# Performance work log

Measured on AMD Instinct MI355X. Metric: run time of the kernel, lower is better.

## Reference

```python
import jax, jax.numpy as jnp
import numpy as np

N, Q, D = 8, 900, 256
HB, WB = 200, 200
L, NH, P = 6, 8, 4
HD = D // NH
FF = 512
NCLS, NBOX = 10, 8
ODIM = NCLS + NBOX
THRESH = 0.5
OFFSET_SCALE = 1.0
SCALE = 1.0 / float(np.sqrt(HD))


def _ln(x, g, b, eps=1e-5):
    m = jnp.mean(x, axis=-1, keepdims=True)
    v = jnp.mean((x - m) ** 2, axis=-1, keepdims=True)
    return (x - m) * jax.lax.rsqrt(v + eps) * g + b


def _mha(x, Wq, bq, Wk, bk, Wv, bv, Wo, bo):
    q = (x @ Wq + bq).reshape(N, Q, NH, HD)
    k = (x @ Wk + bk).reshape(N, Q, NH, HD)
    v = (x @ Wv + bv).reshape(N, Q, NH, HD)
    att = jax.nn.softmax(jnp.einsum('bqhd,bkhd->bhqk', q, k) * SCALE, axis=-1)
    o = jnp.einsum('bhqk,bkhd->bqhd', att, v).reshape(N, Q, D)
    return o @ Wo + bo


def _deform(q, ref, bev, dv_W, dv_b, off_W, off_b, aw_W, aw_b, do_W, do_b):
    # value projection of BEV map: (N, HW, D) -> (N, NH, HW, HD)
    val = (bev @ dv_W + dv_b).reshape(N, HB * WB, NH, HD).transpose(0, 2, 1, 3)
    off = (q @ off_W + off_b).reshape(N, Q, NH, P, 2)
    aw = jax.nn.softmax((q @ aw_W + aw_b).reshape(N, Q, NH, P), axis=-1)
    # ref: (N,Q,1,2) pixel coords -> broadcast to (N,Q,NH,P,2)
    loc = ref[:, :, :, None, :] + off * OFFSET_SCALE
    x = jnp.clip(loc[..., 0], 0.0, WB - 1.0)
    y = jnp.clip(loc[..., 1], 0.0, HB - 1.0)
    x0 = jnp.floor(x)
    y0 = jnp.floor(y)
    x1 = jnp.minimum(x0 + 1.0, WB - 1.0)
    y1 = jnp.minimum(y0 + 1.0, HB - 1.0)
    wx = (x - x0).transpose(0, 2, 1, 3)[..., None]  # (N,NH,Q,P,1)
    wy = (y - y0).transpose(0, 2, 1, 3)[..., None]

    def gather(ix, iy):
        idx = (iy * WB + ix).astype(jnp.int32)               # (N,Q,NH,P)
        idx = idx.transpose(0, 2, 1, 3).reshape(N, NH, Q * P, 1)
        g = jnp.take_along_axis(val, idx, axis=2)            # (N,NH,Q*P,HD)
        return g.reshape(N, NH, Q, P, HD)

    samp = (gather(x0, y0) * (1 - wx) * (1 - wy)
            + gather(x1, y0) * wx * (1 - wy)
            + gather(x0, y1) * (1 - wx) * wy
            + gather(x1, y1) * wx * wy)                      # (N,NH,Q,P,HD)
    awt = aw.transpose(0, 2, 1, 3)                           # (N,NH,Q,P)
    out = jnp.einsum('bhqp,bhqpd->bqhd', awt, samp).reshape(N, Q, D)
    return out @ do_W + do_b


def _ref_points():
    # n_sample=Q points evenly spread over the HBxWB grid, pixel coords, unnormalized
    idx = jnp.round(jnp.linspace(0.0, HB * WB - 1.0, Q)).astype(jnp.int32)
    x = (idx % WB).astype(jnp.float32)
    y = (idx // WB).astype(jnp.float32)
    rp = jnp.stack([x, y], axis=-1)                          # (Q,2)
    return jnp.broadcast_to(rp[None, :, None, :], (N, Q, 1, 2))


def _det(x, W1, b1, W2, b2):
    h = jax.nn.relu(x @ W1 + b1)
    o = h @ W2 + b2
    return jnp.concatenate([jax.nn.sigmoid(o[..., :NCLS]), o[..., NCLS:]], axis=-1)


def setup_inputs() -> dict:
    key = jax.random.key(0)
    ks = iter(jax.random.split(key, 48))

    def w(shape, s=0.02):
        return jax.random.normal(next(ks), shape, jnp.float32) * s

    inp = {
        'bev_features': jax.random.normal(next(ks), (N, HB * WB, D), jnp.float32),
        'pos_emb': w((Q, D), 1.0),
        'Wq': w((L, D, D)), 'bq': jnp.zeros((L, D), jnp.float32),
        'Wk': w((L, D, D)), 'bk': jnp.zeros((L, D), jnp.float32),
        'Wv': w((L, D, D)), 'bv': jnp.zeros((L, D), jnp.float32),
        'Wo': w((L, D, D)), 'bo': jnp.zeros((L, D), jnp.float32),
        'ln1_g': jnp.ones((L, D), jnp.float32), 'ln1_b': jnp.zeros((L, D), jnp.float32),
        'ln2_g': jnp.ones((L, D), jnp.float32), 'ln2_b': jnp.zeros((L, D), jnp.float32),
        'ln3_g': jnp.ones((L, D), jnp.float32), 'ln3_b': jnp.zeros((L, D), jnp.float32),
        'dv_W': w((L, D, D)), 'dv_b': jnp.zeros((L, D), jnp.float32),
        'off_W': w((L, D, NH * P * 2), 0.01), 'off_b': jnp.zeros((L, NH * P * 2), jnp.float32),
        'aw_W': w((L, D, NH * P), 0.01), 'aw_b': jnp.zeros((L, NH * P), jnp.float32),
        'do_W': w((L, D, D)), 'do_b': jnp.zeros((L, D), jnp.float32),
        'f1_W': w((L, D, FF)), 'f1_b': jnp.zeros((L, FF), jnp.float32),
        'f2_W': w((L, FF, D)), 'f2_b': jnp.zeros((L, D), jnp.float32),
        'det_W1': w((D, D)), 'det_b1': jnp.zeros((D,), jnp.float32),
        'det_W2': w((D, ODIM)), 'det_b2': jnp.zeros((ODIM,), jnp.float32),
    }
    return inp


def reference(bev_features, pos_emb, Wq, bq, Wk, bk, Wv, bv, Wo, bo,
              ln1_g, ln1_b, ln2_g, ln2_b, ln3_g, ln3_b,
              dv_W, dv_b, off_W, off_b, aw_W, aw_b, do_W, do_b,
              f1_W, f1_b, f2_W, f2_b, det_W1, det_b1, det_W2, det_b2):
    queries = jnp.broadcast_to(pos_emb[None], (N, Q, D))
    ref = _ref_points()
    output = queries
    layer_results = []
    for i in range(L):
        x = output + queries
        a = _mha(x, Wq[i], bq[i], Wk[i], bk[i], Wv[i], bv[i], Wo[i], bo[i])
        x2 = _ln(x + a, ln1_g[i], ln1_b[i])
        d = _deform(x2, ref, bev_features, dv_W[i], dv_b[i], off_W[i], off_b[i],
                    aw_W[i], aw_b[i], do_W[i], do_b[i])
        x3 = _ln(x2 + d, ln2_g[i], ln2_b[i])
        f = jax.nn.relu(x3 @ f1_W[i] + f1_b[i]) @ f2_W[i] + f2_b[i]
        output = _ln(x3 + f, ln3_g[i], ln3_b[i])
        layer_results.append(_det(output, det_W1, det_b1, det_W2, det_b2))
    layer_results = jnp.stack(layer_results, axis=0)   # (L,N,Q,ODIM)
    detections = layer_results[-1]
    track_mask = detections[..., 0] >= THRESH
    return output, detections, track_mask, layer_results
```

## Files before the change

kernel.cpp:

```cpp
#include <hip/hip_runtime.h>
#include <hip/hip_bf16.h>
#include <math.h>

#define N 8
#define Q 900
#define D 256
#define HB 200
#define WB 200
#define L 6
#define NH 8
#define P 4
#define HD 32
#define FF 512
#define NCLS 10
#define ODIM 18
#define HW (HB*WB)
#define NQ (N*Q)
#define NQD (NQ*D)
#define QD (Q*D)
#define SCALE 0.17677669529663687f

typedef __attribute__((ext_vector_type(4))) float f32x4;
typedef __attribute__((ext_vector_type(8))) short short8v;

__device__ __forceinline__ short bf16_of(float f) {
  __hip_bfloat16 h = __float2bfloat16(f);
  return __builtin_bit_cast(short, h);
}

#define TM 64
#define TN 64
#define KC 128

template <int ACT>
__global__ __launch_bounds__(256) void gemm_kernel(
    const float* __restrict__ A, const float* __restrict__ B,
    const float* __restrict__ bias, float* __restrict__ C,
    int M, int K, int Nc) {
  __shared__ float AsT[KC][TM + 4];
  __shared__ float Bs[KC][TN + 4];
  const int tid = threadIdx.x;
  const int tx = tid & 15, ty = tid >> 4;
  const int m0 = blockIdx.x * TM, n0 = blockIdx.y * TN;

  float c[4][4] = {};

  for (int kc = 0; kc < K; kc += KC) {
    {
      int r = tid >> 2;
      int gr = m0 + r;
      int kb = (tid & 3) * 32;
#pragma unroll
      for (int q = 0; q < 8; ++q) {
        int k = kb + q * 4;
        float4 av = make_float4(0.f, 0.f, 0.f, 0.f);
        if (gr < M) av = *(const float4*)(A + (size_t)gr * K + kc + k);
        AsT[k + 0][r] = av.x; AsT[k + 1][r] = av.y;
        AsT[k + 2][r] = av.z; AsT[k + 3][r] = av.w;
      }
    }
    {
#pragma unroll
      for (int i = 0; i < 8; ++i) {
        int idx = i * 256 + tid;
        int kr = idx >> 4;
        int c4 = (idx & 15) * 4;
        *(float4*)&Bs[kr][c4] = *(const float4*)(B + (size_t)(kc + kr) * Nc + n0 + c4);
      }
    }
    __syncthreads();
#pragma unroll 8
    for (int kk = 0; kk < KC; ++kk) {
      float4 av = *(const float4*)&AsT[kk][ty * 4];
      float4 bv = *(const float4*)&Bs[kk][tx * 4];
      c[0][0] += av.x * bv.x; c[0][1] += av.x * bv.y; c[0][2] += av.x * bv.z; c[0][3] += av.x * bv.w;
      c[1][0] += av.y * bv.x; c[1][1] += av.y * bv.y; c[1][2] += av.y * bv.z; c[1][3] += av.y * bv.w;
      c[2][0] += av.z * bv.x; c[2][1] += av.z * bv.y; c[2][2] += av.z * bv.z; c[2][3] += av.z * bv.w;
      c[3][0] += av.w * bv.x; c[3][1] += av.w * bv.y; c[3][2] += av.w * bv.z; c[3][3] += av.w * bv.w;
    }
    __syncthreads();
  }

#pragma unroll
  for (int i = 0; i < 4; ++i) {
    int row = m0 + ty * 4 + i;
    if (row >= M) continue;
#pragma unroll
    for (int j = 0; j < 4; ++j) {
      int col = n0 + tx * 4 + j;
      float v = c[i][j] + bias[col];
      if (ACT == 1) v = fmaxf(v, 0.f);
      C[(size_t)row * Nc + col] = v;
    }
  }
}

__global__ __launch_bounds__(256) void gemm_qkv_kernel(
    const float* __restrict__ outp, const float* __restrict__ pos,
    const float* __restrict__ Wq, const float* __restrict__ bq,
    const float* __restrict__ Wk, const float* __restrict__ bk,
    const float* __restrict__ Wv, const float* __restrict__ bv,
    unsigned short* __restrict__ Oq, unsigned short* __restrict__ Ok,
    unsigned short* __restrict__ Ov) {
  __shared__ float AsT[KC][TM + 4];
  __shared__ float Bs[KC][TN + 4];
  const int tid = threadIdx.x;
  const int tx = tid & 15, ty = tid >> 4;
  const int m0 = blockIdx.x * TM;
  const int wsel = blockIdx.y >> 2;
  const int n0 = (blockIdx.y & 3) * TN;
  const float* B = (wsel == 0) ? Wq : (wsel == 1) ? Wk : Wv;
  const float* bias = (wsel == 0) ? bq : (wsel == 1) ? bk : bv;
  unsigned short* C = (wsel == 0) ? Oq : (wsel == 1) ? Ok : Ov;

  float c[4][4] = {};

  for (int kc = 0; kc < D; kc += KC) {
    {
      int r = tid >> 2;
      int gr = m0 + r;
      int kb = (tid & 3) * 32;
      const float* ar = outp + (size_t)gr * D + kc;
      const float* pr = pos + (size_t)(gr % Q) * D + kc;
#pragma unroll
      for (int q = 0; q < 8; ++q) {
        int k = kb + q * 4;
        float4 av = make_float4(0.f, 0.f, 0.f, 0.f);
        if (gr < NQ) {
          float4 ov = *(const float4*)(ar + k);
          float4 pv = *(const float4*)(pr + k);
          av.x = ov.x + pv.x; av.y = ov.y + pv.y; av.z = ov.z + pv.z; av.w = ov.w + pv.w;
        }
        AsT[k + 0][r] = av.x; AsT[k + 1][r] = av.y;
        AsT[k + 2][r] = av.z; AsT[k + 3][r] = av.w;
      }
    }
    {
#pragma unroll
      for (int i = 0; i < 8; ++i) {
        int idx = i * 256 + tid;
        int kr = idx >> 4;
        int c4 = (idx & 15) * 4;
        *(float4*)&Bs[kr][c4] = *(const float4*)(B + (size_t)(kc + kr) * D + n0 + c4);
      }
    }
    __syncthreads();
#pragma unroll 8
    for (int kk = 0; kk < KC; ++kk) {
      float4 av = *(const float4*)&AsT[kk][ty * 4];
      float4 bv4 = *(const float4*)&Bs[kk][tx * 4];
      c[0][0] += av.x * bv4.x; c[0][1] += av.x * bv4.y; c[0][2] += av.x * bv4.z; c[0][3] += av.x * bv4.w;
      c[1][0] += av.y * bv4.x; c[1][1] += av.y * bv4.y; c[1][2] += av.y * bv4.z; c[1][3] += av.y * bv4.w;
      c[2][0] += av.z * bv4.x; c[2][1] += av.z * bv4.y; c[2][2] += av.z * bv4.z; c[2][3] += av.z * bv4.w;
      c[3][0] += av.w * bv4.x; c[3][1] += av.w * bv4.y; c[3][2] += av.w * bv4.z; c[3][3] += av.w * bv4.w;
    }
    __syncthreads();
  }

#pragma unroll
  for (int i = 0; i < 4; ++i) {
    int row = m0 + ty * 4 + i;
    if (row >= NQ) continue;
    ushort4 o4;
    o4.x = (unsigned short)bf16_of(c[i][0] + bias[n0 + tx * 4 + 0]);
    o4.y = (unsigned short)bf16_of(c[i][1] + bias[n0 + tx * 4 + 1]);
    o4.z = (unsigned short)bf16_of(c[i][2] + bias[n0 + tx * 4 + 2]);
    o4.w = (unsigned short)bf16_of(c[i][3] + bias[n0 + tx * 4 + 3]);
    *(ushort4*)(C + (size_t)row * D + n0 + tx * 4) = o4;
  }
}

#define TMT 64
template <int ACT>
__global__ __launch_bounds__(256) void gemm_thin_kernel(
    const float* __restrict__ A, const float* __restrict__ B,
    const float* __restrict__ bias, float* __restrict__ C,
    int M, int K, int Nc) {
  __shared__ float AsT[KC][TMT + 4];
  __shared__ float Bs[KC][16 + 2];
  const int tid = threadIdx.x;
  const int tx = tid & 15, ty = tid >> 4;
  const int m0 = blockIdx.x * TMT, n0 = blockIdx.y * 16;

  float c[4] = {};

  for (int kc = 0; kc < K; kc += KC) {
    {
      int r = tid >> 2;
      int gr = m0 + r;
      int kb = (tid & 3) * 32;
#pragma unroll
      for (int q = 0; q < 8; ++q) {
        int k = kb + q * 4;
        float4 av = make_float4(0.f, 0.f, 0.f, 0.f);
        if (gr < M) av = *(const float4*)(A + (size_t)gr * K + kc + k);
        AsT[k + 0][r] = av.x; AsT[k + 1][r] = av.y;
        AsT[k + 2][r] = av.z; AsT[k + 3][r] = av.w;
      }
    }
    {
#pragma unroll
      for (int i = 0; i < 8; ++i) {
        int idx = i * 256 + tid;
        int kr = idx >> 4;
        int cc = idx & 15;
        int gc = n0 + cc;
        Bs[kr][cc] = (gc < Nc) ? B[(size_t)(kc + kr) * Nc + gc] : 0.f;
      }
    }
    __syncthreads();
#pragma unroll 8
    for (int kk = 0; kk < KC; ++kk) {
      float4 av = *(const float4*)&AsT[kk][ty * 4];
      float bv = Bs[kk][tx];
      c[0] += av.x * bv; c[1] += av.y * bv; c[2] += av.z * bv; c[3] += av.w * bv;
    }
    __syncthreads();
  }

  int col = n0 + tx;
  if (col < Nc) {
    float bs = bias[col];
#pragma unroll
    for (int i = 0; i < 4; ++i) {
      int row = m0 + ty * 4 + i;
      if (row < M) {
        float v = c[i] + bs;
        if (ACT == 2 && col < NCLS) v = 1.f / (1.f + expf(-v));
        C[(size_t)row * Nc + col] = v;
      }
    }
  }
}

__global__ __launch_bounds__(256) void gemm_offaw_kernel(
    const float* __restrict__ A,
    const float* __restrict__ offW, const float* __restrict__ offb,
    const float* __restrict__ awW, const float* __restrict__ awb,
    float* __restrict__ offC, float* __restrict__ awC) {
  __shared__ float AsT[KC][TMT + 4];
  __shared__ float Bs[KC][16 + 2];
  const int tid = threadIdx.x;
  const int tx = tid & 15, ty = tid >> 4;
  const int m0 = blockIdx.x * TMT;
  const bool isOff = blockIdx.y < 4;
  const int n0 = isOff ? blockIdx.y * 16 : (blockIdx.y - 4) * 16;
  const int Nc = isOff ? 64 : 32;
  const float* B = isOff ? offW : awW;
  const float* bias = isOff ? offb : awb;
  float* C = isOff ? offC : awC;

  float c[4] = {};

  for (int kc = 0; kc < D; kc += KC) {
    {
      int r = tid >> 2;
      int gr = m0 + r;
      int kb = (tid & 3) * 32;
#pragma unroll
      for (int q = 0; q < 8; ++q) {
        int k = kb + q * 4;
        float4 av = make_float4(0.f, 0.f, 0.f, 0.f);
        if (gr < NQ) av = *(const float4*)(A + (size_t)gr * D + kc + k);
        AsT[k + 0][r] = av.x; AsT[k + 1][r] = av.y;
        AsT[k + 2][r] = av.z; AsT[k + 3][r] = av.w;
      }
    }
    {
#pragma unroll
      for (int i = 0; i < 8; ++i) {
        int idx = i * 256 + tid;
        int kr = idx >> 4;
        int cc = idx & 15;
        Bs[kr][cc] = B[(size_t)(kc + kr) * Nc + n0 + cc];
      }
    }
    __syncthreads();
#pragma unroll 8
    for (int kk = 0; kk < KC; ++kk) {
      float4 av = *(const float4*)&AsT[kk][ty * 4];
      float bv = Bs[kk][tx];
      c[0] += av.x * bv; c[1] += av.y * bv; c[2] += av.z * bv; c[3] += av.w * bv;
    }
    __syncthreads();
  }

  int col = n0 + tx;
  float bs = bias[col];
#pragma unroll
  for (int i = 0; i < 4; ++i) {
    int row = m0 + ty * 4 + i;
    if (row < NQ) C[(size_t)row * Nc + col] = c[i] + bs;
  }
}

__global__ __launch_bounds__(256) void attn_kernel(
    const unsigned short* __restrict__ qg, const unsigned short* __restrict__ kg,
    const unsigned short* __restrict__ vg, float* __restrict__ og) {
  const int n = blockIdx.z, h = blockIdx.y;
  const int wv = threadIdx.x >> 6;
  const int lane = threadIdx.x & 63;
  const int g = lane >> 4;
  const int c = lane & 15;
  const int q0 = blockIdx.x * 64 + wv * 16;

  const unsigned short* qb = qg + (size_t)n * Q * D + h * HD;
  const unsigned short* kb = kg + (size_t)n * Q * D + h * HD;
  const unsigned short* vb = vg + (size_t)n * Q * D + h * HD;

  short8v qf = {};
  {
    int qr = q0 + c;
    if (qr < Q) qf = *(const short8v*)(qb + (size_t)qr * D + g * 8);
  }

  const float SC2 = SCALE * 1.4426950408889634f;
  float m2 = -1e30f, l = 0.f;
  f32x4 acc0 = {0.f, 0.f, 0.f, 0.f}, acc1 = {0.f, 0.f, 0.f, 0.f};

  for (int kt0 = 0; kt0 < Q; kt0 += 64) {
    float s[16];
#pragma unroll
    for (int t = 0; t < 4; ++t) {
      short8v kf = {};
      int kr = kt0 + t * 16 + c;
      if (kr < Q) kf = *(const short8v*)(kb + (size_t)kr * D + g * 8);
      f32x4 d = __builtin_amdgcn_mfma_f32_16x16x32_bf16(kf, qf, (f32x4){0.f, 0.f, 0.f, 0.f}, 0, 0, 0);
#pragma unroll
      for (int r = 0; r < 4; ++r) s[t * 4 + r] = d[r];
    }
#pragma unroll
    for (int t = 0; t < 4; ++t)
#pragma unroll
      for (int r = 0; r < 4; ++r) {
        int key = kt0 + t * 16 + g * 4 + r;
        s[t * 4 + r] = (key < Q) ? s[t * 4 + r] * SC2 : -1e30f;
      }
    float tm = s[0];
#pragma unroll
    for (int j = 1; j < 16; ++j) tm = fmaxf(tm, s[j]);
    tm = fmaxf(tm, __shfl_xor(tm, 16));
    tm = fmaxf(tm, __shfl_xor(tm, 32));
    float m2n = fmaxf(m2, tm);
    float corr = exp2f(m2 - m2n);
    m2 = m2n;
    float ps = 0.f;
#pragma unroll
    for (int j = 0; j < 16; ++j) { s[j] = exp2f(s[j] - m2); ps += s[j]; }
    ps += __shfl_xor(ps, 16);
    ps += __shfl_xor(ps, 32);
    l = l * corr + ps;
    float cr0 = __shfl(corr, g * 4 + 0);
    float cr1 = __shfl(corr, g * 4 + 1);
    float cr2 = __shfl(corr, g * 4 + 2);
    float cr3 = __shfl(corr, g * 4 + 3);
    acc0[0] *= cr0; acc0[1] *= cr1; acc0[2] *= cr2; acc0[3] *= cr3;
    acc1[0] *= cr0; acc1[1] *= cr1; acc1[2] *= cr2; acc1[3] *= cr3;

#pragma unroll
    for (int pr = 0; pr < 2; ++pr) {
      short8v pa, v0 = {}, v1 = {};
#pragma unroll
      for (int j = 0; j < 8; ++j) pa[j] = bf16_of(s[pr * 8 + j]);
#pragma unroll
      for (int j = 0; j < 8; ++j) {
        int key = kt0 + (pr * 2 + (j >> 2)) * 16 + g * 4 + (j & 3);
        if (key < Q) {
          const unsigned short* vp = vb + (size_t)key * D;
          v0[j] = (short)vp[c];
          v1[j] = (short)vp[c + 16];
        }
      }
      acc0 = __builtin_amdgcn_mfma_f32_16x16x32_bf16(pa, v0, acc0, 0, 0, 0);
      acc1 = __builtin_amdgcn_mfma_f32_16x16x32_bf16(pa, v1, acc1, 0, 0, 0);
    }
  }

  float inv = 1.f / l;
  float iv[4];
#pragma unroll
  for (int r = 0; r < 4; ++r) iv[r] = __shfl(inv, g * 4 + r);
#pragma unroll
  for (int r = 0; r < 4; ++r) {
    int qr = q0 + g * 4 + r;
    if (qr < Q) {
      float* op = og + (size_t)(n * Q + qr) * D + h * HD;
      op[c] = acc0[r] * iv[r];
      op[c + 16] = acc1[r] * iv[r];
    }
  }
}

__global__ __launch_bounds__(256) void ln_add_kernel(
    const float* __restrict__ A, const float* __restrict__ Bp,
    const float* __restrict__ g, const float* __restrict__ b,
    float* __restrict__ out) {
  const int wave = threadIdx.x >> 6;
  const int lane = threadIdx.x & 63;
  const int row = blockIdx.x * 4 + wave;
  const size_t base = (size_t)row * D + lane * 4;
  float4 a4 = *(const float4*)(A + base);
  float4 b4 = *(const float4*)(Bp + base);
  float v0 = a4.x + b4.x, v1 = a4.y + b4.y, v2 = a4.z + b4.z, v3 = a4.w + b4.w;
  float sum = v0 + v1 + v2 + v3;
#pragma unroll
  for (int off = 1; off < 64; off <<= 1) sum += __shfl_xor(sum, off);
  float mean = sum * (1.f / D);
  float d0 = v0 - mean, d1 = v1 - mean, d2 = v2 - mean, d3 = v3 - mean;
  float vsum = d0 * d0 + d1 * d1 + d2 * d2 + d3 * d3;
#pragma unroll
  for (int off = 1; off < 64; off <<= 1) vsum += __shfl_xor(vsum, off);
  float inv_std = 1.0f / sqrtf(vsum * (1.f / D) + 1e-5f);
  float4 g4 = *(const float4*)(g + lane * 4);
  float4 bb4 = *(const float4*)(b + lane * 4);
  float4 o4;
  o4.x = d0 * inv_std * g4.x + bb4.x;
  o4.y = d1 * inv_std * g4.y + bb4.y;
  o4.z = d2 * inv_std * g4.z + bb4.z;
  o4.w = d3 * inv_std * g4.w + bb4.w;
  *(float4*)(out + base) = o4;
}

__global__ __launch_bounds__(256) void ln_add3_kernel(
    const float* __restrict__ A, const float* __restrict__ pos,
    const float* __restrict__ Bp,
    const float* __restrict__ g, const float* __restrict__ b,
    float* __restrict__ out) {
  const int wave = threadIdx.x >> 6;
  const int lane = threadIdx.x & 63;
  const int row = blockIdx.x * 4 + wave;
  const size_t base = (size_t)row * D + lane * 4;
  const size_t pbase = (size_t)(row % Q) * D + lane * 4;
  float4 a4 = *(const float4*)(A + base);
  float4 p4 = *(const float4*)(pos + pbase);
  float4 b4 = *(const float4*)(Bp + base);
  float x0 = a4.x + p4.x, x1 = a4.y + p4.y, x2 = a4.z + p4.z, x3 = a4.w + p4.w;
  float v0 = x0 + b4.x, v1 = x1 + b4.y, v2 = x2 + b4.z, v3 = x3 + b4.w;
  float sum = v0 + v1 + v2 + v3;
#pragma unroll
  for (int off = 1; off < 64; off <<= 1) sum += __shfl_xor(sum, off);
  float mean = sum * (1.f / D);
  float d0 = v0 - mean, d1 = v1 - mean, d2 = v2 - mean, d3 = v3 - mean;
  float vsum = d0 * d0 + d1 * d1 + d2 * d2 + d3 * d3;
#pragma unroll
  for (int off = 1; off < 64; off <<= 1) vsum += __shfl_xor(vsum, off);
  float inv_std = 1.0f / sqrtf(vsum * (1.f / D) + 1e-5f);
  float4 g4 = *(const float4*)(g + lane * 4);
  float4 bb4 = *(const float4*)(b + lane * 4);
  float4 o4;
  o4.x = d0 * inv_std * g4.x + bb4.x;
  o4.y = d1 * inv_std * g4.y + bb4.y;
  o4.z = d2 * inv_std * g4.z + bb4.z;
  o4.w = d3 * inv_std * g4.w + bb4.w;
  *(float4*)(out + base) = o4;
}

__global__ __launch_bounds__(256) void deform_kernel(
    const float* __restrict__ bev, const float* __restrict__ offB,
    const float* __restrict__ awB, const float* __restrict__ dvW,
    const float* __restrict__ dvb, float* __restrict__ dtmp) {
  const int bq0 = blockIdx.x * 4;
  const int n = bq0 / Q;
  const int t = threadIdx.x;

  __shared__ float aw_s[4][NH * P];
  __shared__ int   idx_s[4][NH * P * 4];
  __shared__ float w_s[4][NH * P * 4];
  __shared__ float agg_s[4][NH][D];
  __shared__ float red_s[4][4][D];

  if (t < 128) {
    int qq = t >> 5, e = t & 31;
    int bq = bq0 + qq;
    int qi = bq - n * Q;
    float tq = __fmul_rn((float)qi, 44.492767333984375f);
    int ir = (int)rintf(tq);
    float rx = (float)(ir % WB);
    float ry = (float)(ir / WB);
    float ox = offB[(size_t)bq * 64 + e * 2 + 0];
    float oy = offB[(size_t)bq * 64 + e * 2 + 1];
    float lx = fminf(fmaxf(rx + ox, 0.f), (float)(WB - 1));
    float ly = fminf(fmaxf(ry + oy, 0.f), (float)(HB - 1));
    float x0 = floorf(lx), y0 = floorf(ly);
    float x1 = fminf(x0 + 1.f, (float)(WB - 1));
    float y1 = fminf(y0 + 1.f, (float)(HB - 1));
    float wx = lx - x0, wy = ly - y0;
    int b4 = e * 4;
    idx_s[qq][b4 + 0] = (int)y0 * WB + (int)x0; w_s[qq][b4 + 0] = (1.f - wx) * (1.f - wy);
    idx_s[qq][b4 + 1] = (int)y0 * WB + (int)x1; w_s[qq][b4 + 1] = wx * (1.f - wy);
    idx_s[qq][b4 + 2] = (int)y1 * WB + (int)x0; w_s[qq][b4 + 2] = (1.f - wx) * wy;
    idx_s[qq][b4 + 3] = (int)y1 * WB + (int)x1; w_s[qq][b4 + 3] = wx * wy;
  } else if (t < 160) {
    int idx = t - 128;
    int qq = idx >> 3, hh = idx & 7;
    const float* ap = awB + (size_t)(bq0 + qq) * 32 + hh * P;
    float l0 = ap[0], l1 = ap[1], l2 = ap[2], l3 = ap[3];
    float mx = fmaxf(fmaxf(l0, l1), fmaxf(l2, l3));
    float e0 = expf(l0 - mx), e1 = expf(l1 - mx), e2 = expf(l2 - mx), e3 = expf(l3 - mx);
    float inv = 1.f / (e0 + e1 + e2 + e3);
    aw_s[qq][hh * P + 0] = e0 * inv; aw_s[qq][hh * P + 1] = e1 * inv;
    aw_s[qq][hh * P + 2] = e2 * inv; aw_s[qq][hh * P + 3] = e3 * inv;
  }
  __syncthreads();

  {
    const float* bevn = bev + (size_t)n * HW * D;
    const int wv = t >> 6, lane = t & 63;
    const int c4 = lane * 4;
#pragma unroll
    for (int u = 0; u < 8; ++u) {
      int pid = wv + u * 4;
      int qq = pid >> 3, h = pid & 7;
      f32x4 acc = {0.f, 0.f, 0.f, 0.f};
#pragma unroll
      for (int p = 0; p < P; ++p) {
        int e = h * P + p;
        float aw = aw_s[qq][e];
        const int* ix = &idx_s[qq][e * 4];
        const float* wsp = &w_s[qq][e * 4];
        float4 g0 = *(const float4*)(bevn + (size_t)ix[0] * D + c4);
        float4 g1 = *(const float4*)(bevn + (size_t)ix[1] * D + c4);
        float4 g2 = *(const float4*)(bevn + (size_t)ix[2] * D + c4);
        float4 g3 = *(const float4*)(bevn + (size_t)ix[3] * D + c4);
        acc[0] += aw * (wsp[0] * g0.x + wsp[1] * g1.x + wsp[2] * g2.x + wsp[3] * g3.x);
        acc[1] += aw * (wsp[0] * g0.y + wsp[1] * g1.y + wsp[2] * g2.y + wsp[3] * g3.y);
        acc[2] += aw * (wsp[0] * g0.z + wsp[1] * g1.z + wsp[2] * g2.z + wsp[3] * g3.z);
        acc[3] += aw * (wsp[0] * g0.w + wsp[1] * g1.w + wsp[2] * g2.w + wsp[3] * g3.w);
      }
      *(f32x4*)&agg_s[qq][h][c4] = acc;
    }
  }
  __syncthreads();

  {
    const int chunk = t >> 6;
    const int col4 = t & 63;
    const int tt0 = col4 * 4;
    const int h = tt0 >> 5;
    f32x4 p[4] = {{0.f,0.f,0.f,0.f},{0.f,0.f,0.f,0.f},{0.f,0.f,0.f,0.f},{0.f,0.f,0.f,0.f}};
#pragma unroll 4
    for (int dd4 = 0; dd4 < 64; dd4 += 4) {
      int dd = chunk * 64 + dd4;
      float4 w0 = *(const float4*)(dvW + (size_t)(dd + 0) * D + tt0);
      float4 w1 = *(const float4*)(dvW + (size_t)(dd + 1) * D + tt0);
      float4 w2 = *(const float4*)(dvW + (size_t)(dd + 2) * D + tt0);
      float4 w3 = *(const float4*)(dvW + (size_t)(dd + 3) * D + tt0);
#pragma unroll
      for (int qq = 0; qq < 4; ++qq) {
        float4 a = *(const float4*)&agg_s[qq][h][dd];
        p[qq][0] += a.x * w0.x + a.y * w1.x + a.z * w2.x + a.w * w3.x;
        p[qq][1] += a.x * w0.y + a.y * w1.y + a.z * w2.y + a.w * w3.y;
        p[qq][2] += a.x * w0.z + a.y * w1.z + a.z * w2.z + a.w * w3.z;
        p[qq][3] += a.x * w0.w + a.y * w1.w + a.z * w2.w + a.w * w3.w;
      }
    }
#pragma unroll
    for (int qq = 0; qq < 4; ++qq) *(f32x4*)&red_s[qq][chunk][tt0] = p[qq];
  }
  __syncthreads();
  {
    float bs = dvb[t];
#pragma unroll
    for (int qq = 0; qq < 4; ++qq) {
      dtmp[(size_t)(bq0 + qq) * D + t] =
          bs + red_s[qq][0][t] + red_s[qq][1][t] + red_s[qq][2][t] + red_s[qq][3][t];
    }
  }
}

__global__ void bcast_q_kernel(const float* __restrict__ pos, float* __restrict__ out) {
  for (size_t i = (size_t)blockIdx.x * blockDim.x + threadIdx.x; i < (size_t)NQD;
       i += (size_t)gridDim.x * blockDim.x)
    out[i] = pos[i % QD];
}
__global__ void finalize_kernel(const float* __restrict__ lr5, float* __restrict__ det,
                                float* __restrict__ mask) {
  int i = blockIdx.x * blockDim.x + threadIdx.x;
  if (i < NQ * ODIM) det[i] = lr5[i];
  if (i < NQ) mask[i] = (lr5[(size_t)i * ODIM] >= 0.5f) ? 1.0f : 0.0f;
}

extern "C" void kernel_launch(void* const* d_in, const int* in_sizes, int n_in,
                              void* d_out, int out_size, void* d_ws, size_t ws_size,
                              hipStream_t stream) {
  const float* bev  = (const float*)d_in[0];
  const float* pos  = (const float*)d_in[1];
  const float* Wq   = (const float*)d_in[2];  const float* bq  = (const float*)d_in[3];
  const float* Wk   = (const float*)d_in[4];  const float* bk  = (const float*)d_in[5];
  const float* Wv   = (const float*)d_in[6];  const float* bv  = (const float*)d_in[7];
  const float* Wo   = (const float*)d_in[8];  const float* bo  = (const float*)d_in[9];
  const float* ln1g = (const float*)d_in[10]; const float* ln1b = (const float*)d_in[11];
  const float* ln2g = (const float*)d_in[12]; const float* ln2b = (const float*)d_in[13];
  const float* ln3g = (const float*)d_in[14]; const float* ln3b = (const float*)d_in[15];
  const float* dvW  = (const float*)d_in[16]; const float* dvb = (const float*)d_in[17];
  const float* offW = (const float*)d_in[18]; const float* offb = (const float*)d_in[19];
  const float* awW  = (const float*)d_in[20]; const float* awb = (const float*)d_in[21];
  const float* doW  = (const float*)d_in[22]; const float* dob = (const float*)d_in[23];
  const float* f1W  = (const float*)d_in[24]; const float* f1b = (const float*)d_in[25];
  const float* f2W  = (const float*)d_in[26]; const float* f2b = (const float*)d_in[27];
  const float* dW1  = (const float*)d_in[28]; const float* db1 = (const float*)d_in[29];
  const float* dW2  = (const float*)d_in[30]; const float* db2 = (const float*)d_in[31];

  float* w = (float*)d_ws;
  float* b0 = w + 0 * (size_t)NQD;
  float* b1 = w + 1 * (size_t)NQD;
  float* b2 = w + 2 * (size_t)NQD;
  float* b3 = w + 3 * (size_t)NQD;
  float* ffh = b1;
  float* offB = b0;
  float* awB  = b0 + (size_t)NQ * 64;
  unsigned short* qb16 = (unsigned short*)b1;
  unsigned short* kb16 = (unsigned short*)b1 + NQD;
  unsigned short* vb16 = (unsigned short*)b2;

  float* out_output = (float*)d_out;
  float* out_det    = out_output + (size_t)NQD;
  float* out_mask   = out_det + (size_t)NQ * ODIM;
  float* out_lr     = out_mask + (size_t)NQ;

  const dim3 blk256(256);
  const dim3 qkvGrid((NQ + TM - 1) / TM, 12);
  const dim3 gemmGridD((NQ + TM - 1) / TM, D / TN);
  const dim3 gemmGridFF((NQ + TM - 1) / TM, FF / TN);
  const dim3 offawGrid((NQ + TMT - 1) / TMT, 6);
  const dim3 thinGridDet((NQ + TMT - 1) / TMT, 2);
  const dim3 attnGrid((Q + 63) / 64, NH, N);
  const dim3 lnGrid(NQ / 4);
  const dim3 defGrid(NQ / 4);
  const int ewGrid = 1024;

  bcast_q_kernel<<<ewGrid, blk256, 0, stream>>>(pos, out_output);

  for (int i = 0; i < L; ++i) {
    const size_t wDD = (size_t)i * D * D;
    gemm_qkv_kernel<<<qkvGrid, blk256, 0, stream>>>(out_output, pos,
        Wq + wDD, bq + (size_t)i * D, Wk + wDD, bk + (size_t)i * D,
        Wv + wDD, bv + (size_t)i * D, qb16, kb16, vb16);
    attn_kernel<<<attnGrid, blk256, 0, stream>>>(qb16, kb16, vb16, b0);
    gemm_kernel<0><<<gemmGridD, blk256, 0, stream>>>(b0, Wo + wDD, bo + (size_t)i * D, b1, NQ, D, D);
    ln_add3_kernel<<<lnGrid, blk256, 0, stream>>>(out_output, pos, b1,
        ln1g + (size_t)i * D, ln1b + (size_t)i * D, b2);
    gemm_offaw_kernel<<<offawGrid, blk256, 0, stream>>>(b2,
        offW + (size_t)i * D * 64, offb + (size_t)i * 64,
        awW + (size_t)i * D * 32, awb + (size_t)i * 32, offB, awB);
    deform_kernel<<<defGrid, blk256, 0, stream>>>(bev, offB, awB, dvW + wDD, dvb + (size_t)i * D, b3);
    gemm_kernel<0><<<gemmGridD, blk256, 0, stream>>>(b3, doW + wDD, dob + (size_t)i * D, b1, NQ, D, D);
    ln_add_kernel<<<lnGrid, blk256, 0, stream>>>(b2, b1, ln2g + (size_t)i * D, ln2b + (size_t)i * D, b0);
    gemm_kernel<1><<<gemmGridFF, blk256, 0, stream>>>(b0, f1W + (size_t)i * D * FF, f1b + (size_t)i * FF, ffh, NQ, D, FF);
    gemm_kernel<0><<<gemmGridD, blk256, 0, stream>>>(ffh, f2W + (size_t)i * FF * D, f2b + (size_t)i * D, b3, NQ, FF, D);
    ln_add_kernel<<<lnGrid, blk256, 0, stream>>>(b0, b3, ln3g + (size_t)i * D, ln3b + (size_t)i * D, out_output);
    gemm_kernel<1><<<gemmGridD, blk256, 0, stream>>>(out_output, dW1, db1, b1, NQ, D, D);
    gemm_thin_kernel<2><<<thinGridDet, blk256, 0, stream>>>(b1, dW2, db2, out_lr + (size_t)i * NQ * ODIM, NQ, D, ODIM);
  }

  finalize_kernel<<<(NQ * ODIM + 255) / 256, blk256, 0, stream>>>(out_lr + (size_t)(L - 1) * NQ * ODIM,
                                                                  out_det, out_mask);
}
```

Measured before the change: 2.418 ms.

## Split deform into gather and per-head projection GEMM; shrink attention blocks

The deformable sampling kernel no longer does the value projection in shared memory. It writes per-head aggregated BEV features to a new workspace buffer, and a separate tiled GEMM kernel then applies the per-head slice of the value projection. This is meant to relieve the large shared-memory footprint and the weak projection loop of the fused kernel. The cost is an extra global round trip of an NQ×NH×D buffer and one extra launch. The attention kernel also moves from 256-thread blocks of four waves to single-wave blocks to give more blocks and better occupancy.

```diff
diff --git a/kernel.cpp b/kernel.cpp
--- a/kernel.cpp
+++ b/kernel.cpp
@@ -294,15 +294,70 @@
   }
 }
 
-__global__ __launch_bounds__(256) void attn_kernel(
+__global__ __launch_bounds__(256) void dproj_kernel(
+    const float* __restrict__ agg, const float* __restrict__ dvW,
+    const float* __restrict__ dvb, float* __restrict__ dtmp) {
+  __shared__ float AsT[KC][TMT + 4];
+  __shared__ float Bs[KC][16 + 2];
+  const int tid = threadIdx.x;
+  const int tx = tid & 15, ty = tid >> 4;
+  const int m0 = blockIdx.x * TMT;
+  const int n0 = blockIdx.y * 16;
+  const int h = blockIdx.z;
+  const int ldA = NH * D;
+
+  float c[4] = {};
+
+  for (int kc = 0; kc < D; kc += KC) {
+    {
+      int r = tid >> 2;
+      int gr = m0 + r;
+      int kb = (tid & 3) * 32;
+#pragma unroll
+      for (int q = 0; q < 8; ++q) {
+        int k = kb + q * 4;
+        float4 av = make_float4(0.f, 0.f, 0.f, 0.f);
+        if (gr < NQ) av = *(const float4*)(agg + (size_t)gr * ldA + h * D + kc + k);
+        AsT[k + 0][r] = av.x; AsT[k + 1][r] = av.y;
+        AsT[k + 2][r] = av.z; AsT[k + 3][r] = av.w;
+      }
+    }
+    {
+#pragma unroll
+      for (int i = 0; i < 8; ++i) {
+        int idx = i * 256 + tid;
+        int kr = idx >> 4;
+        int cc = idx & 15;
+        Bs[kr][cc] = dvW[(size_t)(kc + kr) * D + h * HD + n0 + cc];
+      }
+    }
+    __syncthreads();
+#pragma unroll 8
+    for (int kk = 0; kk < KC; ++kk) {
+      float4 av = *(const float4*)&AsT[kk][ty * 4];
+      float bv = Bs[kk][tx];
+      c[0] += av.x * bv; c[1] += av.y * bv; c[2] += av.z * bv; c[3] += av.w * bv;
+    }
+    __syncthreads();
+  }
+
+  int col = h * HD + n0 + tx;
+  float bs = dvb[col];
+#pragma unroll
+  for (int i = 0; i < 4; ++i) {
+    int row = m0 + ty * 4 + i;
+    if (row < NQ) dtmp[(size_t)row * D + col] = c[i] + bs;
+  }
+}
+
+__global__ __launch_bounds__(64) void attn_kernel(
     const unsigned short* __restrict__ qg, const unsigned short* __restrict__ kg,
     const unsigned short* __restrict__ vg, float* __restrict__ og) {
   const int n = blockIdx.z, h = blockIdx.y;
-  const int wv = threadIdx.x >> 6;
-  const int lane = threadIdx.x & 63;
+  const int lane = threadIdx.x;
   const int g = lane >> 4;
   const int c = lane & 15;
-  const int q0 = blockIdx.x * 64 + wv * 16;
+  const int q0 = blockIdx.x * 16;
 
   const unsigned short* qb = qg + (size_t)n * Q * D + h * HD;
   const unsigned short* kb = kg + (size_t)n * Q * D + h * HD;
@@ -455,10 +510,9 @@
   *(float4*)(out + base) = o4;
 }
 
-__global__ __launch_bounds__(256) void deform_kernel(
+__global__ __launch_bounds__(256) void deform_gather_kernel(
     const float* __restrict__ bev, const float* __restrict__ offB,
-    const float* __restrict__ awB, const float* __restrict__ dvW,
-    const float* __restrict__ dvb, float* __restrict__ dtmp) {
+    const float* __restrict__ awB, float* __restrict__ agg) {
   const int bq0 = blockIdx.x * 4;
   const int n = bq0 / Q;
   const int t = threadIdx.x;
@@ -466,8 +520,6 @@
   __shared__ float aw_s[4][NH * P];
   __shared__ int   idx_s[4][NH * P * 4];
   __shared__ float w_s[4][NH * P * 4];
-  __shared__ float agg_s[4][NH][D];
-  __shared__ float red_s[4][4][D];
 
   if (t < 128) {
     int qq = t >> 5, e = t & 31;
@@ -527,43 +579,7 @@
         acc[2] += aw * (wsp[0] * g0.z + wsp[1] * g1.z + wsp[2] * g2.z + wsp[3] * g3.z);
         acc[3] += aw * (wsp[0] * g0.w + wsp[1] * g1.w + wsp[2] * g2.w + wsp[3] * g3.w);
       }
-      *(f32x4*)&agg_s[qq][h][c4] = acc;
-    }
-  }
-  __syncthreads();
-
-  {
-    const int chunk = t >> 6;
-    const int col4 = t & 63;
-    const int tt0 = col4 * 4;
-    const int h = tt0 >> 5;
-    f32x4 p[4] = {{0.f,0.f,0.f,0.f},{0.f,0.f,0.f,0.f},{0.f,0.f,0.f,0.f},{0.f,0.f,0.f,0.f}};
-#pragma unroll 4
-    for (int dd4 = 0; dd4 < 64; dd4 += 4) {
-      int dd = chunk * 64 + dd4;
-      float4 w0 = *(const float4*)(dvW + (size_t)(dd + 0) * D + tt0);
-      float4 w1 = *(const float4*)(dvW + (size_t)(dd + 1) * D + tt0);
-      float4 w2 = *(const float4*)(dvW + (size_t)(dd + 2) * D + tt0);
-      float4 w3 = *(const float4*)(dvW + (size_t)(dd + 3) * D + tt0);
-#pragma unroll
-      for (int qq = 0; qq < 4; ++qq) {
-        float4 a = *(const float4*)&agg_s[qq][h][dd];
-        p[qq][0] += a.x * w0.x + a.y * w1.x + a.z * w2.x + a.w * w3.x;
-        p[qq][1] += a.x * w0.y + a.y * w1.y + a.z * w2.y + a.w * w3.y;
-        p[qq][2] += a.x * w0.z + a.y * w1.z + a.z * w2.z + a.w * w3.z;
-        p[qq][3] += a.x * w0.w + a.y * w1.w + a.z * w2.w + a.w * w3.w;
-      }
-    }
-#pragma unroll
-    for (int qq = 0; qq < 4; ++qq) *(f32x4*)&red_s[qq][chunk][tt0] = p[qq];
-  }
-  __syncthreads();
-  {
-    float bs = dvb[t];
-#pragma unroll
-    for (int qq = 0; qq < 4; ++qq) {
-      dtmp[(size_t)(bq0 + qq) * D + t] =
-          bs + red_s[qq][0][t] + red_s[qq][1][t] + red_s[qq][2][t] + red_s[qq][3][t];
+      *(f32x4*)(agg + ((size_t)(bq0 + qq) * NH + h) * D + c4) = acc;
     }
   }
 }
@@ -606,6 +622,7 @@
   float* b1 = w + 1 * (size_t)NQD;
   float* b2 = w + 2 * (size_t)NQD;
   float* b3 = w + 3 * (size_t)NQD;
+  float* agg = w + 4 * (size_t)NQD;
   float* ffh = b1;
   float* offB = b0;
   float* awB  = b0 + (size_t)NQ * 64;
@@ -619,12 +636,14 @@
   float* out_lr     = out_mask + (size_t)NQ;
 
   const dim3 blk256(256);
+  const dim3 blk64(64);
   const dim3 qkvGrid((NQ + TM - 1) / TM, 12);
   const dim3 gemmGridD((NQ + TM - 1) / TM, D / TN);
   const dim3 gemmGridFF((NQ + TM - 1) / TM, FF / TN);
   const dim3 offawGrid((NQ + TMT - 1) / TMT, 6);
   const dim3 thinGridDet((NQ + TMT - 1) / TMT, 2);
-  const dim3 attnGrid((Q + 63) / 64, NH, N);
+  const dim3 dprojGrid((NQ + TMT - 1) / TMT, 2, NH);
+  const dim3 attnGrid((Q + 15) / 16, NH, N);
   const dim3 lnGrid(NQ / 4);
   const dim3 defGrid(NQ / 4);
   const int ewGrid = 1024;
@@ -636,14 +655,15 @@
     gemm_qkv_kernel<<<qkvGrid, blk256, 0, stream>>>(out_output, pos,
         Wq + wDD, bq + (size_t)i * D, Wk + wDD, bk + (size_t)i * D,
         Wv + wDD, bv + (size_t)i * D, qb16, kb16, vb16);
-    attn_kernel<<<attnGrid, blk256, 0, stream>>>(qb16, kb16, vb16, b0);
+    attn_kernel<<<attnGrid, blk64, 0, stream>>>(qb16, kb16, vb16, b0);
     gemm_kernel<0><<<gemmGridD, blk256, 0, stream>>>(b0, Wo + wDD, bo + (size_t)i * D, b1, NQ, D, D);
     ln_add3_kernel<<<lnGrid, blk256, 0, stream>>>(out_output, pos, b1,
         ln1g + (size_t)i * D, ln1b + (size_t)i * D, b2);
     gemm_offaw_kernel<<<offawGrid, blk256, 0, stream>>>(b2,
         offW + (size_t)i * D * 64, offb + (size_t)i * 64,
         awW + (size_t)i * D * 32, awb + (size_t)i * 32, offB, awB);
-    deform_kernel<<<defGrid, blk256, 0, stream>>>(bev, offB, awB, dvW + wDD, dvb + (size_t)i * D, b3);
+    deform_gather_kernel<<<defGrid, blk256, 0, stream>>>(bev, offB, awB, agg);
+    dproj_kernel<<<dprojGrid, blk256, 0, stream>>>(agg, dvW + wDD, dvb + (size_t)i * D, b3);
     gemm_kernel<0><<<gemmGridD, blk256, 0, stream>>>(b3, doW + wDD, dob + (size_t)i * D, b1, NQ, D, D);
     ln_add_kernel<<<lnGrid, blk256, 0, stream>>>(b2, b1, ln2g + (size_t)i * D, ln2b + (size_t)i * D, b0);
     gemm_kernel<1><<<gemmGridFF, blk256, 0, stream>>>(b0, f1W + (size_t)i * D * FF, f1b + (size_t)i * FF, ffh, NQ, D, FF);
```

Result: slower. 2.578 ms (+6.6%).
